# Optimization experiments

Measured on AMD Instinct MI355X. Metric: run time of the kernel, lower is better.

## Reference

```python
import jax, jax.numpy as jnp
import numpy as np

D = 768          # n_embd
I = 3072         # moe_intermediate_size (4 * n_embd)
E = 8            # n_routed_experts
K = 2            # num_experts_per_tok
LIMIT = 10.0     # swiglu_limit
VOCAB = 32768


def setup_inputs() -> dict:
    key = jax.random.key(0)
    ks = jax.random.split(key, 10)
    s = 0.02
    return {
        "x": jax.random.normal(ks[0], (1, 2048, D), dtype=jnp.float32),
        "input_ids": jax.random.randint(ks[1], (1, 2048), 0, VOCAB, dtype=jnp.int64),
        "gate_w": jax.random.normal(ks[2], (D, E), dtype=jnp.float32) * s,
        "gate_bias": jnp.zeros((E,), dtype=jnp.float32),
        "w1": jax.random.normal(ks[3], (E, D, I), dtype=jnp.float32) * s,
        "w2": jax.random.normal(ks[4], (E, I, D), dtype=jnp.float32) * s,
        "w3": jax.random.normal(ks[5], (E, D, I), dtype=jnp.float32) * s,
        "w1s": jax.random.normal(ks[6], (D, I), dtype=jnp.float32) * s,
        "w2s": jax.random.normal(ks[7], (I, D), dtype=jnp.float32) * s,
        "w3s": jax.random.normal(ks[8], (D, I), dtype=jnp.float32) * s,
    }


def _expert(xf, W1, W2, W3):
    # SwiGLU with asymmetric clamping, as in DeepSeekExpert (swiglu_limit > 0)
    gate = jnp.minimum(xf @ W1, LIMIT)               # clamp max only
    up = jnp.clip(xf @ W3, -LIMIT, LIMIT)            # clamp both sides
    return (jax.nn.silu(gate) * up) @ W2


def reference(x, input_ids, gate_w, gate_bias, w1, w2, w3, w1s, w2s, w3s):
    B, T, _ = x.shape
    flat = x.reshape(-1, D)                           # [N, D], N = B*T
    N = flat.shape[0]

    # gating: sqrtsoftplus scoring
    scores = jnp.sqrt(jax.nn.softplus(flat @ gate_w))  # [N, E]
    routed_scores = scores + gate_bias                 # gate_bias used only for topk selection
    _, indices = jax.lax.top_k(routed_scores, K)       # [N, K]

    weights = jnp.take_along_axis(scores, indices, axis=1)  # [N, K]
    # norm_topk_prob=True; routed_scaling_factor=1.0
    weights = weights / jnp.clip(weights.sum(axis=-1, keepdims=True), 1e-6)

    # dense combine matrix [N, E] (jit-friendly dispatch/combine)
    combine = jnp.zeros((N, E), dtype=weights.dtype)
    combine = combine.at[jnp.arange(N)[:, None], indices].add(weights)

    # shared expert on all tokens
    y = _expert(flat, w1s, w2s, w3s)                   # [N, D]

    # routed experts: batched grouped GEMM over all tokens, then weighted combine
    gate_h = jnp.minimum(jnp.einsum('td,edi->eti', flat, w1), LIMIT)   # [E, N, I]
    up_h = jnp.clip(jnp.einsum('td,edi->eti', flat, w3), -LIMIT, LIMIT)
    h = jax.nn.silu(gate_h) * up_h                     # [E, N, I]
    out_e = jnp.einsum('eti,eid->etd', h, w2)          # [E, N, D]
    routed = jnp.einsum('etd,te->td', out_e, combine)  # [N, D]

    return (y + routed).reshape(B, T, D)
```

## Files before the change

### kernel.cpp

```cpp
#include <hip/hip_runtime.h>


#define D_ 768
#define I_ 3072
#define E_ 8
#define NTOK 2048
#define NPMAX 5120
#define MAXTILES 40
#define NSHT 16
#define ROWS (NTOK + NPMAX)
#define SPLITK 2
#define KS_ (I_ / SPLITK)

#define NT2 5184

typedef __bf16 bf16x8 __attribute__((ext_vector_type(8)));
typedef float floatx4 __attribute__((ext_vector_type(4)));

#define GLOAD_LDS16(g, l) __builtin_amdgcn_global_load_lds( \
    (const __attribute__((address_space(1))) void*)(g),     \
    (__attribute__((address_space(3))) void*)(l), 16, 0, 0)

__device__ __forceinline__ unsigned short f2b(float f) {
    unsigned int u = __float_as_uint(f);
    u += 0x7fffu + ((u >> 16) & 1u);
    return (unsigned short)(u >> 16);
}


__global__ __launch_bounds__(256) void prep_kernel(
    const float* __restrict__ x, const float* __restrict__ gw,
    const float* __restrict__ gbias,
    const float* __restrict__ w1, const float* __restrict__ w3,
    const float* __restrict__ w1s, const float* __restrict__ w3s,
    unsigned short* __restrict__ xb,
    unsigned short* __restrict__ w1b, unsigned short* __restrict__ w3b,
    unsigned short* __restrict__ w1sb, unsigned short* __restrict__ w3sb,
    int* __restrict__ idx, float* __restrict__ wts) {
    __shared__ float t[64][65];
    int b = blockIdx.x, tid = threadIdx.x;
    if (b < 10368) {
        const float* s; unsigned short* d;
        int z = b / 576, r = b % 576;
        int bx = r % 48, by = r / 48;
        const int R = D_, C = I_;
        if (z < 8)       { s = w1 + (size_t)z * D_ * I_;       d = w1b + (size_t)z * D_ * I_; }
        else if (z < 16) { s = w3 + (size_t)(z - 8) * D_ * I_; d = w3b + (size_t)(z - 8) * D_ * I_; }
        else if (z == 16){ s = w1s; d = w1sb; }
        else             { s = w3s; d = w3sb; }
        int c0 = bx * 64, r0 = by * 64;
#pragma unroll
        for (int j = 0; j < 4; j++) {
            int slot = tid + j * 256;
            int rr = slot >> 4, c4 = (slot & 15) * 4;
            float4 v = *(const float4*)(s + (size_t)(r0 + rr) * C + c0 + c4);
            t[rr][c4] = v.x; t[rr][c4 + 1] = v.y; t[rr][c4 + 2] = v.z; t[rr][c4 + 3] = v.w;
        }
        __syncthreads();
#pragma unroll
        for (int j = 0; j < 2; j++) {
            int slot = tid + j * 256;
            int c = slot >> 3, rs = (slot & 7) * 8;
            unsigned short o[8] __attribute__((aligned(16)));
#pragma unroll
            for (int i = 0; i < 8; i++) o[i] = f2b(t[rs + i][c]);
            *(int4*)(d + (size_t)(c0 + c) * R + r0 + rs) = *(const int4*)o;
        }
    } else if (b < 11904) {
        int gid = (b - 10368) * 256 + tid;
        float4 v = *(const float4*)(x + (size_t)gid * 4);
        ushort4 o;
        o.x = f2b(v.x); o.y = f2b(v.y); o.z = f2b(v.z); o.w = f2b(v.w);
        *(ushort4*)(xb + (size_t)gid * 4) = o;
    } else {
        int tok = (b - 11904) * 4 + (tid >> 6);
        int lane = tid & 63;
        float z[E_];
#pragma unroll
        for (int e = 0; e < E_; e++) z[e] = 0.f;
        const float* xr = x + (size_t)tok * D_;
        for (int j = lane; j < D_; j += 64) {
            float xv = xr[j];
            const float* g = gw + (size_t)j * E_;
#pragma unroll
            for (int e = 0; e < E_; e++) z[e] += xv * g[e];
        }
#pragma unroll
        for (int off = 32; off > 0; off >>= 1)
#pragma unroll
            for (int e = 0; e < E_; e++) z[e] += __shfl_down(z[e], off, 64);
        if (lane == 0) {
            float s[E_], r[E_];
#pragma unroll
            for (int e = 0; e < E_; e++) {
                float zz = z[e];
                float sp = zz > 0.f ? zz + log1pf(expf(-zz)) : log1pf(expf(zz));
                s[e] = sqrtf(sp);
                r[e] = s[e] + gbias[e];
            }
            int i0 = 0;
            for (int e = 1; e < E_; e++) if (r[e] > r[i0]) i0 = e;
            int i1 = (i0 == 0) ? 1 : 0;
            for (int e = 0; e < E_; e++) if (e != i0 && r[e] > r[i1]) i1 = e;
            float w0 = s[i0], w1v = s[i1];
            float inv = 1.f / fmaxf(w0 + w1v, 1e-6f);
            idx[2 * tok] = i0; idx[2 * tok + 1] = i1;
            wts[2 * tok] = w0 * inv; wts[2 * tok + 1] = w1v * inv;
        }
    }
}


__global__ void route_build_kernel(const int* __restrict__ idx,
                                   const float* __restrict__ wts,
                                   int* __restrict__ pair_token,
                                   float* __restrict__ pair_w,
                                   int* __restrict__ pos_of,
                                   int* __restrict__ tiles) {
    __shared__ int cnt[E_], seg[E_], cur[E_];
    int tid = threadIdx.x;
    if (tid < E_) { cnt[tid] = 0; cur[tid] = 0; }
    __syncthreads();
    for (int p = tid; p < NTOK * 2; p += 256) atomicAdd(&cnt[idx[p]], 1);
    __syncthreads();
    if (tid == 0) {
        int off = 0, nt = 0;
        for (int e = 0; e < E_; e++) {
            seg[e] = off;
            int te = (cnt[e] + 127) >> 7;
            for (int j = 0; j < te; j++) {
                tiles[nt * 2] = e; tiles[nt * 2 + 1] = off + j * 128; nt++;
            }
            off += te * 128;
        }
        for (; nt < MAXTILES; nt++) { tiles[nt * 2] = -1; tiles[nt * 2 + 1] = 0; }
    }
    for (int p = tid; p < NPMAX; p += 256) pair_token[p] = -1;
    __syncthreads();
    for (int p = tid; p < NTOK * 2; p += 256) {
        int e = idx[p];
        int r = atomicAdd(&cur[e], 1);
        int pos = seg[e] + r;
        pair_token[pos] = p >> 1;
        pair_w[pos] = wts[p];
        pos_of[p] = pos;
    }
}


__launch_bounds__(256)
__global__ void gemm_act_kernel(const unsigned short* __restrict__ xb,
                                const unsigned short* __restrict__ w1sb,
                                const unsigned short* __restrict__ w3sb,
                                const unsigned short* __restrict__ w1b,
                                const unsigned short* __restrict__ w3b,
                                const int* __restrict__ tiles,
                                const int* __restrict__ pair_token,
                                unsigned short* __restrict__ act,
                                const float* __restrict__ w2,
                                const float* __restrict__ w2s,
                                unsigned short* __restrict__ w2b,
                                unsigned short* __restrict__ w2sb) {
    __shared__ __align__(16) unsigned short smem[128 * 64 + 64 * 64 + 64 * 64];
    unsigned short* As  = smem;
    unsigned short* Bs1 = smem + 128 * 64;
    unsigned short* Bs3 = smem + 128 * 64 + 64 * 64;

    int bxi = blockIdx.x, byi = blockIdx.y;
    int tid = threadIdx.x;

    if (byi % 3) {
        int slot = byi - byi / 3 - 1;
        int b2 = slot * 48 + bxi;
        if (b2 >= NT2) return;
        float (*t)[65] = (float(*)[65])smem;
        const float* s; unsigned short* dst;
        int z = b2 / 576, r = b2 % 576;
        int tx = r % 12, ty = r / 12;
        const int R = I_, C = D_;
        if (z < 8) { s = w2 + (size_t)z * I_ * D_; dst = w2b + (size_t)z * I_ * D_; }
        else       { s = w2s; dst = w2sb; }
        int c0 = tx * 64, r0 = ty * 64;
#pragma unroll
        for (int j = 0; j < 4; j++) {
            int sl = tid + j * 256;
            int rr = sl >> 4, c4 = (sl & 15) * 4;
            float4 v = *(const float4*)(s + (size_t)(r0 + rr) * C + c0 + c4);
            t[rr][c4] = v.x; t[rr][c4 + 1] = v.y; t[rr][c4 + 2] = v.z; t[rr][c4 + 3] = v.w;
        }
        __syncthreads();
#pragma unroll
        for (int j = 0; j < 2; j++) {
            int sl = tid + j * 256;
            int c = sl >> 3, rs = (sl & 7) * 8;
            unsigned short o[8] __attribute__((aligned(16)));
#pragma unroll
            for (int i = 0; i < 8; i++) o[i] = f2b(t[rs + i][c]);
            *(int4*)(dst + (size_t)(c0 + c) * R + r0 + rs) = *(const int4*)o;
        }
        return;
    }

    int mt = byi / 3;
    const unsigned short *B1, *B3;
    int m0; bool routed;
    if (mt < NSHT) {
        B1 = w1sb; B3 = w3sb; m0 = mt * 128; routed = false;
    } else {
        int e = tiles[(mt - NSHT) * 2];
        if (e < 0) return;
        m0 = NTOK + tiles[(mt - NSHT) * 2 + 1];
        B1 = w1b + (size_t)e * I_ * D_; B3 = w3b + (size_t)e * I_ * D_;
        routed = true;
    }
    int n0 = bxi * 64;
    int lane = tid & 63, wave = tid >> 6;
    int wm = (wave & 1) * 64, wn = (wave >> 1) * 32;
    int l15 = lane & 15, quad = lane >> 4;

    int rl = lane >> 3;
    int ph = lane & 7;
    int lg = ph ^ rl;
    const unsigned short* asrc[4];
#pragma unroll
    for (int j = 0; j < 4; j++) {
        int r = j * 32 + wave * 8 + rl;
        int tok;
        if (routed) { tok = pair_token[m0 - NTOK + r]; if (tok < 0) tok = 0; }
        else tok = m0 + r;
        asrc[j] = xb + (size_t)tok * D_ + lg * 8;
    }
    const unsigned short *b1src[2], *b3src[2];
#pragma unroll
    for (int j = 0; j < 2; j++) {
        int r = j * 32 + wave * 8 + rl;
        b1src[j] = B1 + (size_t)(n0 + r) * D_ + lg * 8;
        b3src[j] = B3 + (size_t)(n0 + r) * D_ + lg * 8;
    }
    unsigned short *ldA[4], *ldB1[2], *ldB3[2];
#pragma unroll
    for (int j = 0; j < 4; j++) ldA[j] = As + (j * 32 + wave * 8) * 64;
#pragma unroll
    for (int j = 0; j < 2; j++) {
        ldB1[j] = Bs1 + (j * 32 + wave * 8) * 64;
        ldB3[j] = Bs3 + (j * 32 + wave * 8) * 64;
    }

    floatx4 acc1[4][2] = {}; floatx4 acc3[4][2] = {};
    int sx = (l15 & 7);

    for (int k0 = 0; k0 < D_; k0 += 64) {
        __syncthreads();
#pragma unroll
        for (int j = 0; j < 4; j++) GLOAD_LDS16(asrc[j] + k0, ldA[j]);
#pragma unroll
        for (int j = 0; j < 2; j++) {
            GLOAD_LDS16(b1src[j] + k0, ldB1[j]);
            GLOAD_LDS16(b3src[j] + k0, ldB3[j]);
        }
        __syncthreads();

#pragma unroll
        for (int kk = 0; kk < 2; kk++) {
            int pq = ((kk * 4 + quad) ^ sx) * 8;
            bf16x8 af[4], b1f[2], b3f[2];
#pragma unroll
            for (int mi = 0; mi < 4; mi++)
                af[mi] = *(const bf16x8*)(As + (wm + mi * 16 + l15) * 64 + pq);
#pragma unroll
            for (int ni = 0; ni < 2; ni++) {
                b1f[ni] = *(const bf16x8*)(Bs1 + (wn + ni * 16 + l15) * 64 + pq);
                b3f[ni] = *(const bf16x8*)(Bs3 + (wn + ni * 16 + l15) * 64 + pq);
            }
#pragma unroll
            for (int mi = 0; mi < 4; mi++)
#pragma unroll
                for (int ni = 0; ni < 2; ni++) {
                    acc1[mi][ni] = __builtin_amdgcn_mfma_f32_16x16x32_bf16(
                        af[mi], b1f[ni], acc1[mi][ni], 0, 0, 0);
                    acc3[mi][ni] = __builtin_amdgcn_mfma_f32_16x16x32_bf16(
                        af[mi], b3f[ni], acc3[mi][ni], 0, 0, 0);
                }
        }
    }

#pragma unroll
    for (int mi = 0; mi < 4; mi++)
#pragma unroll
        for (int ni = 0; ni < 2; ni++) {
            int col = n0 + wn + ni * 16 + l15;
#pragma unroll
            for (int rr = 0; rr < 4; rr++) {
                int row = m0 + wm + mi * 16 + quad * 4 + rr;
                float g = fminf(acc1[mi][ni][rr], 10.f);
                float u = fminf(fmaxf(acc3[mi][ni][rr], -10.f), 10.f);
                float a = g / (1.f + __expf(-g)) * u;
                act[(size_t)row * I_ + col] = f2b(a);
            }
        }
}


__launch_bounds__(256)
__global__ void gemm_out_kernel(const unsigned short* __restrict__ act,
                                const unsigned short* __restrict__ w2sb,
                                const unsigned short* __restrict__ w2b,
                                const int* __restrict__ tiles,
                                float* __restrict__ outp) {
    __shared__ __align__(16) unsigned short As[128 * 64];
    __shared__ __align__(16) unsigned short Bs[64 * 64];

    int mt = blockIdx.y, ks = blockIdx.z;
    int kbase = ks * KS_;
    const unsigned short* B;
    int m0;
    if (mt < NSHT) {
        B = w2sb; m0 = mt * 128;
    } else {
        int e = tiles[(mt - NSHT) * 2];
        if (e < 0) return;
        m0 = NTOK + tiles[(mt - NSHT) * 2 + 1];
        B = w2b + (size_t)e * I_ * D_;
    }
    float* C = outp + (size_t)ks * ROWS * D_;
    int n0 = blockIdx.x * 64;
    int tid = threadIdx.x;
    int lane = tid & 63, wave = tid >> 6;
    int wm = (wave & 1) * 64, wn = (wave >> 1) * 32;
    int l15 = lane & 15, quad = lane >> 4;

    int rl = lane >> 3, ph = lane & 7, lg = ph ^ rl;
    const unsigned short* asrc[4];
#pragma unroll
    for (int j = 0; j < 4; j++)
        asrc[j] = act + (size_t)(m0 + j * 32 + wave * 8 + rl) * I_ + kbase + lg * 8;
    const unsigned short* bsrc[2];
#pragma unroll
    for (int j = 0; j < 2; j++)
        bsrc[j] = B + (size_t)(n0 + j * 32 + wave * 8 + rl) * I_ + kbase + lg * 8;
    unsigned short *ldA[4], *ldB[2];
#pragma unroll
    for (int j = 0; j < 4; j++) ldA[j] = As + (j * 32 + wave * 8) * 64;
#pragma unroll
    for (int j = 0; j < 2; j++) ldB[j] = Bs + (j * 32 + wave * 8) * 64;

    floatx4 acc[4][2] = {};
    int sx = (l15 & 7);

    for (int k0 = 0; k0 < KS_; k0 += 64) {
        __syncthreads();
#pragma unroll
        for (int j = 0; j < 4; j++) GLOAD_LDS16(asrc[j] + k0, ldA[j]);
#pragma unroll
        for (int j = 0; j < 2; j++) GLOAD_LDS16(bsrc[j] + k0, ldB[j]);
        __syncthreads();

#pragma unroll
        for (int kk = 0; kk < 2; kk++) {
            int pq = ((kk * 4 + quad) ^ sx) * 8;
            bf16x8 af[4], bf[2];
#pragma unroll
            for (int mi = 0; mi < 4; mi++)
                af[mi] = *(const bf16x8*)(As + (wm + mi * 16 + l15) * 64 + pq);
#pragma unroll
            for (int ni = 0; ni < 2; ni++)
                bf[ni] = *(const bf16x8*)(Bs + (wn + ni * 16 + l15) * 64 + pq);
#pragma unroll
            for (int mi = 0; mi < 4; mi++)
#pragma unroll
                for (int ni = 0; ni < 2; ni++)
                    acc[mi][ni] = __builtin_amdgcn_mfma_f32_16x16x32_bf16(
                        af[mi], bf[ni], acc[mi][ni], 0, 0, 0);
        }
    }

#pragma unroll
    for (int mi = 0; mi < 4; mi++)
#pragma unroll
        for (int ni = 0; ni < 2; ni++) {
            int col = n0 + wn + ni * 16 + l15;
#pragma unroll
            for (int rr = 0; rr < 4; rr++) {
                int row = m0 + wm + mi * 16 + quad * 4 + rr;
                C[(size_t)row * D_ + col] = acc[mi][ni][rr];
            }
        }
}


__global__ void combine_kernel(const float* __restrict__ outp,
                               const int* __restrict__ pos_of,
                               const float* __restrict__ pair_w,
                               float* __restrict__ out) {
    int gid = blockIdx.x * 256 + threadIdx.x;
    int t = gid / (D_ / 4);
    int j = (gid % (D_ / 4)) * 4;
    int p0 = pos_of[2 * t], p1 = pos_of[2 * t + 1];
    float w0 = pair_w[p0], w1 = pair_w[p1];
    float a0 = 0.f, a1 = 0.f, a2 = 0.f, a3 = 0.f;
#pragma unroll
    for (int ks = 0; ks < SPLITK; ks++) {
        const float* P = outp + (size_t)ks * ROWS * D_;
        float4 a = *(const float4*)(P + (size_t)t * D_ + j);
        float4 b = *(const float4*)(P + (size_t)(NTOK + p0) * D_ + j);
        float4 c = *(const float4*)(P + (size_t)(NTOK + p1) * D_ + j);
        a0 += a.x + w0 * b.x + w1 * c.x;
        a1 += a.y + w0 * b.y + w1 * c.y;
        a2 += a.z + w0 * b.z + w1 * c.z;
        a3 += a.w + w0 * b.w + w1 * c.w;
    }
    float4 o; o.x = a0; o.y = a1; o.z = a2; o.w = a3;
    *(float4*)(out + (size_t)t * D_ + j) = o;
}


extern "C" void kernel_launch(void* const* d_in, const int* in_sizes, int n_in,
                              void* d_out, int out_size, void* d_ws, size_t ws_size,
                              hipStream_t stream) {
    (void)in_sizes; (void)n_in; (void)out_size; (void)ws_size;
    const float* x   = (const float*)d_in[0];
    const float* gw  = (const float*)d_in[2];
    const float* gb  = (const float*)d_in[3];
    const float* w1  = (const float*)d_in[4];
    const float* w2  = (const float*)d_in[5];
    const float* w3  = (const float*)d_in[6];
    const float* w1s = (const float*)d_in[7];
    const float* w2s = (const float*)d_in[8];
    const float* w3s = (const float*)d_in[9];
    float* out = (float*)d_out;

    char* ws = (char*)d_ws;
    size_t off = 0;
    auto alloc = [&](size_t bytes) {
        size_t o = (off + 255) & ~(size_t)255;
        off = o + bytes;
        return (void*)(ws + o);
    };
    unsigned short* xb   = (unsigned short*)alloc((size_t)NTOK * D_ * 2);
    unsigned short* w1b  = (unsigned short*)alloc((size_t)E_ * I_ * D_ * 2);
    unsigned short* w3b  = (unsigned short*)alloc((size_t)E_ * I_ * D_ * 2);
    unsigned short* w2b  = (unsigned short*)alloc((size_t)E_ * I_ * D_ * 2);
    unsigned short* w1sb = (unsigned short*)alloc((size_t)I_ * D_ * 2);
    unsigned short* w3sb = (unsigned short*)alloc((size_t)I_ * D_ * 2);
    unsigned short* w2sb = (unsigned short*)alloc((size_t)I_ * D_ * 2);
    unsigned short* act  = (unsigned short*)alloc((size_t)ROWS * I_ * 2);
    float* outp = (float*)alloc((size_t)SPLITK * ROWS * D_ * 4);
    int*   idx  = (int*)alloc((size_t)NTOK * 2 * 4);
    float* wts  = (float*)alloc((size_t)NTOK * 2 * 4);
    int*   ptok = (int*)alloc((size_t)NPMAX * 4);
    float* pw   = (float*)alloc((size_t)NPMAX * 4);
    int*   posf = (int*)alloc((size_t)NTOK * 2 * 4);
    int*   tls  = (int*)alloc((size_t)MAXTILES * 2 * 4);

    prep_kernel<<<12416, 256, 0, stream>>>(x, gw, gb, w1, w3, w1s, w3s,
                                           xb, w1b, w3b, w1sb, w3sb, idx, wts);
    route_build_kernel<<<1, 256, 0, stream>>>(idx, wts, ptok, pw, posf, tls);
    gemm_act_kernel<<<dim3(I_ / 64, 168), 256, 0, stream>>>(
        xb, w1sb, w3sb, w1b, w3b, tls, ptok, act, w2, w2s, w2b, w2sb);
    gemm_out_kernel<<<dim3(D_ / 64, NSHT + MAXTILES, SPLITK), 256, 0, stream>>>(
        act, w2sb, w2b, tls, outp);
    combine_kernel<<<NTOK * (D_ / 4) / 256, 256, 0, stream>>>(outp, posf, pw, out);
}
```

Baseline: 461.8 us.

## Overlap weight bf16 conversion with shared and routed GEMMs across kernels

Restructures the pipeline so the large routed-expert weight transposes/conversions run inside the GEMM kernels instead of a big upfront prep kernel. Only the shared-expert weights, x, and gating are converted in prep. The shared GEMM kernel carries the w1/w3 routed conversion plus the routing build, and the routed GEMM kernel carries the w2 conversion. This is meant to hide the memory-bound conversion behind compute and drop a separate launch. It relies on kernel ordering for the dependencies and interleaves conversion blocks with GEMM blocks via block-index mapping.

```diff
diff --git a/kernel.cpp b/kernel.cpp
--- a/kernel.cpp
+++ b/kernel.cpp
@@ -12,8 +12,6 @@
 #define SPLITK 2
 #define KS_ (I_ / SPLITK)
 
-#define NT2 5184
-
 typedef __bf16 bf16x8 __attribute__((ext_vector_type(8)));
 typedef float floatx4 __attribute__((ext_vector_type(4)));
 
@@ -27,53 +25,59 @@
     return (unsigned short)(u >> 16);
 }
 
-
-__global__ __launch_bounds__(256) void prep_kernel(
+__device__ __forceinline__ void transpose_tile(const float* __restrict__ s,
+                                               unsigned short* __restrict__ d,
+                                               int R, int C, int r0, int c0,
+                                               float (*t)[65], int tid) {
+#pragma unroll
+    for (int j = 0; j < 4; j++) {
+        int slot = tid + j * 256;
+        int rr = slot >> 4, c4 = (slot & 15) * 4;
+        float4 v = *(const float4*)(s + (size_t)(r0 + rr) * C + c0 + c4);
+        t[rr][c4] = v.x; t[rr][c4 + 1] = v.y; t[rr][c4 + 2] = v.z; t[rr][c4 + 3] = v.w;
+    }
+    __syncthreads();
+#pragma unroll
+    for (int j = 0; j < 2; j++) {
+        int slot = tid + j * 256;
+        int c = slot >> 3, rs = (slot & 7) * 8;
+        unsigned short o[8] __attribute__((aligned(16)));
+#pragma unroll
+        for (int i = 0; i < 8; i++) o[i] = f2b(t[rs + i][c]);
+        *(int4*)(d + (size_t)(c0 + c) * R + r0 + rs) = *(const int4*)o;
+    }
+}
+
+
+__global__ __launch_bounds__(256) void prep_lite_kernel(
     const float* __restrict__ x, const float* __restrict__ gw,
     const float* __restrict__ gbias,
-    const float* __restrict__ w1, const float* __restrict__ w3,
     const float* __restrict__ w1s, const float* __restrict__ w3s,
+    const float* __restrict__ w2s,
     unsigned short* __restrict__ xb,
-    unsigned short* __restrict__ w1b, unsigned short* __restrict__ w3b,
     unsigned short* __restrict__ w1sb, unsigned short* __restrict__ w3sb,
+    unsigned short* __restrict__ w2sb,
     int* __restrict__ idx, float* __restrict__ wts) {
     __shared__ float t[64][65];
     int b = blockIdx.x, tid = threadIdx.x;
-    if (b < 10368) {
-        const float* s; unsigned short* d;
+    if (b < 1728) {
         int z = b / 576, r = b % 576;
-        int bx = r % 48, by = r / 48;
-        const int R = D_, C = I_;
-        if (z < 8)       { s = w1 + (size_t)z * D_ * I_;       d = w1b + (size_t)z * D_ * I_; }
-        else if (z < 16) { s = w3 + (size_t)(z - 8) * D_ * I_; d = w3b + (size_t)(z - 8) * D_ * I_; }
-        else if (z == 16){ s = w1s; d = w1sb; }
-        else             { s = w3s; d = w3sb; }
-        int c0 = bx * 64, r0 = by * 64;
-#pragma unroll
-        for (int j = 0; j < 4; j++) {
-            int slot = tid + j * 256;
-            int rr = slot >> 4, c4 = (slot & 15) * 4;
-            float4 v = *(const float4*)(s + (size_t)(r0 + rr) * C + c0 + c4);
-            t[rr][c4] = v.x; t[rr][c4 + 1] = v.y; t[rr][c4 + 2] = v.z; t[rr][c4 + 3] = v.w;
-        }
-        __syncthreads();
-#pragma unroll
-        for (int j = 0; j < 2; j++) {
-            int slot = tid + j * 256;
-            int c = slot >> 3, rs = (slot & 7) * 8;
-            unsigned short o[8] __attribute__((aligned(16)));
-#pragma unroll
-            for (int i = 0; i < 8; i++) o[i] = f2b(t[rs + i][c]);
-            *(int4*)(d + (size_t)(c0 + c) * R + r0 + rs) = *(const int4*)o;
-        }
-    } else if (b < 11904) {
-        int gid = (b - 10368) * 256 + tid;
+        if (z < 2) {
+            int bx = r % 48, by = r / 48;
+            transpose_tile(z ? w3s : w1s, z ? w3sb : w1sb, D_, I_,
+                           by * 64, bx * 64, t, tid);
+        } else {
+            int tx = r % 12, ty = r / 12;
+            transpose_tile(w2s, w2sb, I_, D_, ty * 64, tx * 64, t, tid);
+        }
+    } else if (b < 3264) {
+        int gid = (b - 1728) * 256 + tid;
         float4 v = *(const float4*)(x + (size_t)gid * 4);
         ushort4 o;
         o.x = f2b(v.x); o.y = f2b(v.y); o.z = f2b(v.z); o.w = f2b(v.w);
         *(ushort4*)(xb + (size_t)gid * 4) = o;
     } else {
-        int tok = (b - 11904) * 4 + (tid >> 6);
+        int tok = (b - 3264) * 4 + (tid >> 6);
         int lane = tid & 63;
         float z[E_];
 #pragma unroll
@@ -111,123 +115,201 @@
 }
 
 
-__global__ void route_build_kernel(const int* __restrict__ idx,
+__launch_bounds__(256)
+__global__ void gemm_shared_kernel(const unsigned short* __restrict__ xb,
+                                   const unsigned short* __restrict__ w1sb,
+                                   const unsigned short* __restrict__ w3sb,
+                                   unsigned short* __restrict__ act,
+                                   const float* __restrict__ w1,
+                                   const float* __restrict__ w3,
+                                   unsigned short* __restrict__ w1b,
+                                   unsigned short* __restrict__ w3b,
+                                   const int* __restrict__ idx,
                                    const float* __restrict__ wts,
                                    int* __restrict__ pair_token,
                                    float* __restrict__ pair_w,
                                    int* __restrict__ pos_of,
                                    int* __restrict__ tiles) {
-    __shared__ int cnt[E_], seg[E_], cur[E_];
-    int tid = threadIdx.x;
-    if (tid < E_) { cnt[tid] = 0; cur[tid] = 0; }
-    __syncthreads();
-    for (int p = tid; p < NTOK * 2; p += 256) atomicAdd(&cnt[idx[p]], 1);
-    __syncthreads();
-    if (tid == 0) {
-        int off = 0, nt = 0;
-        for (int e = 0; e < E_; e++) {
-            seg[e] = off;
-            int te = (cnt[e] + 127) >> 7;
-            for (int j = 0; j < te; j++) {
-                tiles[nt * 2] = e; tiles[nt * 2 + 1] = off + j * 128; nt++;
-            }
-            off += te * 128;
-        }
-        for (; nt < MAXTILES; nt++) { tiles[nt * 2] = -1; tiles[nt * 2 + 1] = 0; }
-    }
-    for (int p = tid; p < NPMAX; p += 256) pair_token[p] = -1;
-    __syncthreads();
-    for (int p = tid; p < NTOK * 2; p += 256) {
-        int e = idx[p];
-        int r = atomicAdd(&cur[e], 1);
-        int pos = seg[e] + r;
-        pair_token[pos] = p >> 1;
-        pair_w[pos] = wts[p];
-        pos_of[p] = pos;
-    }
-}
-
-
-__launch_bounds__(256)
-__global__ void gemm_act_kernel(const unsigned short* __restrict__ xb,
-                                const unsigned short* __restrict__ w1sb,
-                                const unsigned short* __restrict__ w3sb,
-                                const unsigned short* __restrict__ w1b,
-                                const unsigned short* __restrict__ w3b,
-                                const int* __restrict__ tiles,
-                                const int* __restrict__ pair_token,
-                                unsigned short* __restrict__ act,
-                                const float* __restrict__ w2,
-                                const float* __restrict__ w2s,
-                                unsigned short* __restrict__ w2b,
-                                unsigned short* __restrict__ w2sb) {
     __shared__ __align__(16) unsigned short smem[128 * 64 + 64 * 64 + 64 * 64];
     unsigned short* As  = smem;
     unsigned short* Bs1 = smem + 128 * 64;
     unsigned short* Bs3 = smem + 128 * 64 + 64 * 64;
 
-    int bxi = blockIdx.x, byi = blockIdx.y;
-    int tid = threadIdx.x;
-
-    if (byi % 3) {
-        int slot = byi - byi / 3 - 1;
+    int bxi = blockIdx.x, byi = blockIdx.y, tid = threadIdx.x;
+
+    if (byi == 0) {
+        if (bxi) return;
+        int* cnt = (int*)smem; int* seg = cnt + E_; int* cur = cnt + 2 * E_;
+        if (tid < E_) { cnt[tid] = 0; cur[tid] = 0; }
+        __syncthreads();
+        for (int p = tid; p < NTOK * 2; p += 256) atomicAdd(&cnt[idx[p]], 1);
+        __syncthreads();
+        if (tid == 0) {
+            int off = 0, nt = 0;
+            for (int e = 0; e < E_; e++) {
+                seg[e] = off;
+                int te = (cnt[e] + 127) >> 7;
+                for (int j = 0; j < te; j++) {
+                    tiles[nt * 2] = e; tiles[nt * 2 + 1] = off + j * 128; nt++;
+                }
+                off += te * 128;
+            }
+            for (; nt < MAXTILES; nt++) { tiles[nt * 2] = -1; tiles[nt * 2 + 1] = 0; }
+        }
+        for (int p = tid; p < NPMAX; p += 256) pair_token[p] = -1;
+        __syncthreads();
+        for (int p = tid; p < NTOK * 2; p += 256) {
+            int e = idx[p];
+            int r = atomicAdd(&cur[e], 1);
+            int pos = seg[e] + r;
+            pair_token[pos] = p >> 1;
+            pair_w[pos] = wts[p];
+            pos_of[p] = pos;
+        }
+        return;
+    }
+
+    int t = byi - 1;
+    if (t % 13) {
+        int slot = t - t / 13 - 1;
         int b2 = slot * 48 + bxi;
-        if (b2 >= NT2) return;
-        float (*t)[65] = (float(*)[65])smem;
-        const float* s; unsigned short* dst;
         int z = b2 / 576, r = b2 % 576;
-        int tx = r % 12, ty = r / 12;
-        const int R = I_, C = D_;
-        if (z < 8) { s = w2 + (size_t)z * I_ * D_; dst = w2b + (size_t)z * I_ * D_; }
-        else       { s = w2s; dst = w2sb; }
-        int c0 = tx * 64, r0 = ty * 64;
-#pragma unroll
-        for (int j = 0; j < 4; j++) {
-            int sl = tid + j * 256;
-            int rr = sl >> 4, c4 = (sl & 15) * 4;
-            float4 v = *(const float4*)(s + (size_t)(r0 + rr) * C + c0 + c4);
-            t[rr][c4] = v.x; t[rr][c4 + 1] = v.y; t[rr][c4 + 2] = v.z; t[rr][c4 + 3] = v.w;
-        }
-        __syncthreads();
-#pragma unroll
-        for (int j = 0; j < 2; j++) {
-            int sl = tid + j * 256;
-            int c = sl >> 3, rs = (sl & 7) * 8;
-            unsigned short o[8] __attribute__((aligned(16)));
-#pragma unroll
-            for (int i = 0; i < 8; i++) o[i] = f2b(t[rs + i][c]);
-            *(int4*)(dst + (size_t)(c0 + c) * R + r0 + rs) = *(const int4*)o;
-        }
+        int bx = r % 48, by = r / 48;
+        const float* s; unsigned short* d;
+        if (z < 8) { s = w1 + (size_t)z * D_ * I_;       d = w1b + (size_t)z * D_ * I_; }
+        else       { s = w3 + (size_t)(z - 8) * D_ * I_; d = w3b + (size_t)(z - 8) * D_ * I_; }
+        transpose_tile(s, d, D_, I_, by * 64, bx * 64, (float(*)[65])smem, tid);
         return;
     }
 
-    int mt = byi / 3;
-    const unsigned short *B1, *B3;
-    int m0; bool routed;
-    if (mt < NSHT) {
-        B1 = w1sb; B3 = w3sb; m0 = mt * 128; routed = false;
-    } else {
-        int e = tiles[(mt - NSHT) * 2];
-        if (e < 0) return;
-        m0 = NTOK + tiles[(mt - NSHT) * 2 + 1];
-        B1 = w1b + (size_t)e * I_ * D_; B3 = w3b + (size_t)e * I_ * D_;
-        routed = true;
-    }
+    int mt = t / 13;
+    int m0 = mt * 128;
     int n0 = bxi * 64;
     int lane = tid & 63, wave = tid >> 6;
     int wm = (wave & 1) * 64, wn = (wave >> 1) * 32;
     int l15 = lane & 15, quad = lane >> 4;
 
-    int rl = lane >> 3;
-    int ph = lane & 7;
-    int lg = ph ^ rl;
+    int rl = lane >> 3, ph = lane & 7, lg = ph ^ rl;
+    const unsigned short* asrc[4];
+#pragma unroll
+    for (int j = 0; j < 4; j++)
+        asrc[j] = xb + (size_t)(m0 + j * 32 + wave * 8 + rl) * D_ + lg * 8;
+    const unsigned short *b1src[2], *b3src[2];
+#pragma unroll
+    for (int j = 0; j < 2; j++) {
+        int r = j * 32 + wave * 8 + rl;
+        b1src[j] = w1sb + (size_t)(n0 + r) * D_ + lg * 8;
+        b3src[j] = w3sb + (size_t)(n0 + r) * D_ + lg * 8;
+    }
+    unsigned short *ldA[4], *ldB1[2], *ldB3[2];
+#pragma unroll
+    for (int j = 0; j < 4; j++) ldA[j] = As + (j * 32 + wave * 8) * 64;
+#pragma unroll
+    for (int j = 0; j < 2; j++) {
+        ldB1[j] = Bs1 + (j * 32 + wave * 8) * 64;
+        ldB3[j] = Bs3 + (j * 32 + wave * 8) * 64;
+    }
+
+    floatx4 acc1[4][2] = {}; floatx4 acc3[4][2] = {};
+    int sx = (l15 & 7);
+
+    for (int k0 = 0; k0 < D_; k0 += 64) {
+        __syncthreads();
+#pragma unroll
+        for (int j = 0; j < 4; j++) GLOAD_LDS16(asrc[j] + k0, ldA[j]);
+#pragma unroll
+        for (int j = 0; j < 2; j++) {
+            GLOAD_LDS16(b1src[j] + k0, ldB1[j]);
+            GLOAD_LDS16(b3src[j] + k0, ldB3[j]);
+        }
+        __syncthreads();
+
+#pragma unroll
+        for (int kk = 0; kk < 2; kk++) {
+            int pq = ((kk * 4 + quad) ^ sx) * 8;
+            bf16x8 af[4], b1f[2], b3f[2];
+#pragma unroll
+            for (int mi = 0; mi < 4; mi++)
+                af[mi] = *(const bf16x8*)(As + (wm + mi * 16 + l15) * 64 + pq);
+#pragma unroll
+            for (int ni = 0; ni < 2; ni++) {
+                b1f[ni] = *(const bf16x8*)(Bs1 + (wn + ni * 16 + l15) * 64 + pq);
+                b3f[ni] = *(const bf16x8*)(Bs3 + (wn + ni * 16 + l15) * 64 + pq);
+            }
+#pragma unroll
+            for (int mi = 0; mi < 4; mi++)
+#pragma unroll
+                for (int ni = 0; ni < 2; ni++) {
+                    acc1[mi][ni] = __builtin_amdgcn_mfma_f32_16x16x32_bf16(
+                        af[mi], b1f[ni], acc1[mi][ni], 0, 0, 0);
+                    acc3[mi][ni] = __builtin_amdgcn_mfma_f32_16x16x32_bf16(
+                        af[mi], b3f[ni], acc3[mi][ni], 0, 0, 0);
+                }
+        }
+    }
+
+#pragma unroll
+    for (int mi = 0; mi < 4; mi++)
+#pragma unroll
+        for (int ni = 0; ni < 2; ni++) {
+            int col = n0 + wn + ni * 16 + l15;
+#pragma unroll
+            for (int rr = 0; rr < 4; rr++) {
+                int row = m0 + wm + mi * 16 + quad * 4 + rr;
+                float g = fminf(acc1[mi][ni][rr], 10.f);
+                float u = fminf(fmaxf(acc3[mi][ni][rr], -10.f), 10.f);
+                float a = g / (1.f + __expf(-g)) * u;
+                act[(size_t)row * I_ + col] = f2b(a);
+            }
+        }
+}
+
+
+__launch_bounds__(256)
+__global__ void gemm_routed_kernel(const unsigned short* __restrict__ xb,
+                                   const unsigned short* __restrict__ w1b,
+                                   const unsigned short* __restrict__ w3b,
+                                   const int* __restrict__ tiles,
+                                   const int* __restrict__ pair_token,
+                                   unsigned short* __restrict__ act,
+                                   const float* __restrict__ w2,
+                                   unsigned short* __restrict__ w2b) {
+    __shared__ __align__(16) unsigned short smem[128 * 64 + 64 * 64 + 64 * 64];
+    unsigned short* As  = smem;
+    unsigned short* Bs1 = smem + 128 * 64;
+    unsigned short* Bs3 = smem + 128 * 64 + 64 * 64;
+
+    int bxi = blockIdx.x, byi = blockIdx.y, tid = threadIdx.x;
+    int g = byi / 17, h = byi % 17;
+
+    if (h >= 5) {
+        int slot = g * 12 + (h - 5);
+        int b2 = slot * 48 + bxi;
+        int z = b2 / 576, r = b2 % 576;
+        int tx = r % 12, ty = r / 12;
+        transpose_tile(w2 + (size_t)z * I_ * D_, w2b + (size_t)z * I_ * D_,
+                       I_, D_, ty * 64, tx * 64, (float(*)[65])smem, tid);
+        return;
+    }
+
+    int mt = g * 5 + h;
+    int e = tiles[mt * 2];
+    if (e < 0) return;
+    int m0 = NTOK + tiles[mt * 2 + 1];
+    const unsigned short* B1 = w1b + (size_t)e * I_ * D_;
+    const unsigned short* B3 = w3b + (size_t)e * I_ * D_;
+
+    int n0 = bxi * 64;
+    int lane = tid & 63, wave = tid >> 6;
+    int wm = (wave & 1) * 64, wn = (wave >> 1) * 32;
+    int l15 = lane & 15, quad = lane >> 4;
+
+    int rl = lane >> 3, ph = lane & 7, lg = ph ^ rl;
     const unsigned short* asrc[4];
 #pragma unroll
     for (int j = 0; j < 4; j++) {
         int r = j * 32 + wave * 8 + rl;
-        int tok;
-        if (routed) { tok = pair_token[m0 - NTOK + r]; if (tok < 0) tok = 0; }
-        else tok = m0 + r;
+        int tok = pair_token[m0 - NTOK + r]; if (tok < 0) tok = 0;
         asrc[j] = xb + (size_t)tok * D_ + lg * 8;
     }
     const unsigned short *b1src[2], *b3src[2];
@@ -452,11 +534,12 @@
     int*   posf = (int*)alloc((size_t)NTOK * 2 * 4);
     int*   tls  = (int*)alloc((size_t)MAXTILES * 2 * 4);
 
-    prep_kernel<<<12416, 256, 0, stream>>>(x, gw, gb, w1, w3, w1s, w3s,
-                                           xb, w1b, w3b, w1sb, w3sb, idx, wts);
-    route_build_kernel<<<1, 256, 0, stream>>>(idx, wts, ptok, pw, posf, tls);
-    gemm_act_kernel<<<dim3(I_ / 64, 168), 256, 0, stream>>>(
-        xb, w1sb, w3sb, w1b, w3b, tls, ptok, act, w2, w2s, w2b, w2sb);
+    prep_lite_kernel<<<3776, 256, 0, stream>>>(x, gw, gb, w1s, w3s, w2s,
+                                               xb, w1sb, w3sb, w2sb, idx, wts);
+    gemm_shared_kernel<<<dim3(48, 209), 256, 0, stream>>>(
+        xb, w1sb, w3sb, act, w1, w3, w1b, w3b, idx, wts, ptok, pw, posf, tls);
+    gemm_routed_kernel<<<dim3(48, 136), 256, 0, stream>>>(
+        xb, w1b, w3b, tls, ptok, act, w2, w2b);
     gemm_out_kernel<<<dim3(D_ / 64, NSHT + MAXTILES, SPLITK), 256, 0, stream>>>(
         act, w2sb, w2b, tls, outp);
     combine_kernel<<<NTOK * (D_ / 4) / 256, 256, 0, stream>>>(outp, posf, pw, out);
```

Result: faster. 436.9 us (-5.4%).
